# Kernel tuning notes

Measured on AMD Instinct MI355X. Metric: run time of the kernel, lower is better.

The kernel has to match this reference:

```python
import jax, jax.numpy as jnp
import numpy as np
import math

INPUT_DIM = 1024
EXPANSION = 4
SPARSITY = 0.15
ACT_SPARSITY = 0.1
OUTPUT_DIM = INPUT_DIM * EXPANSION
K = max(1, int(OUTPUT_DIM * ACT_SPARSITY))  # 409
BATCH = 16384


def setup_inputs() -> dict:
    key = jax.random.key(0)
    kx, kw, km = jax.random.split(key, 3)
    x = jax.random.normal(kx, (BATCH, INPUT_DIM), dtype=jnp.float32)
    # sparse random projection buffer, built exactly as in __init__
    w = jax.random.normal(kw, (OUTPUT_DIM, INPUT_DIM), dtype=jnp.float32)
    mask = (jax.random.uniform(km, (OUTPUT_DIM, INPUT_DIM)) < SPARSITY).astype(jnp.float32)
    scale = 1.5 / math.sqrt(INPUT_DIM * SPARSITY)
    projection_weights = w * mask * scale
    return {"x": x, "projection_weights": projection_weights}


def reference(x, projection_weights):
    # data-dependent bipolar rescale: torch uses `if x.min() >= 0`; express with where
    x_bipolar = jnp.where(x.min() >= 0, (x - 0.5) * 2.0, x)
    # [B, D_out] dense projection
    projected = jnp.einsum("bi,oi->bo", x_bipolar, projection_weights)
    # k-WTA: threshold at k-th largest value per row
    top_values, _ = jax.lax.top_k(projected, K)
    threshold = top_values[:, -1:]  # [B, 1]
    mask = (projected >= threshold).astype(projected.dtype)
    encoded = jax.nn.relu(projected) * mask
    # F.normalize(p=2, dim=1): divide by max(norm, eps)
    norm = jnp.sqrt(jnp.sum(encoded * encoded, axis=1, keepdims=True))
    return encoded / jnp.maximum(norm, 1e-12)
```

## Files before the change

### kernel.cpp

```cpp
#include <hip/hip_runtime.h>

#define BATCH   16384
#define IN_DIM  1024
#define OUT_DIM 4096
#define K_TOP   409
#define DELTA_W 6.5e-3f

typedef _Float16 half8  __attribute__((ext_vector_type(8)));
typedef _Float16 half4v __attribute__((ext_vector_type(4)));
typedef float    f32x4  __attribute__((ext_vector_type(4)));

#define WS_XH_OFF   256
#define WS_WH_OFF   (WS_XH_OFF + (size_t)BATCH * IN_DIM * 2)
#define WS_WV_OFF   (WS_WH_OFF + (size_t)OUT_DIM * IN_DIM * 2)
#define WS_WI_OFF   (WS_WV_OFF + (size_t)OUT_DIM * 256 * 4)
#define WS_WN_OFF   (WS_WI_OFF + (size_t)OUT_DIM * 256 * 2)
#define WS_NEEDED   (WS_WV_OFF)
#define WS_NEED3    (WS_WN_OFF + (size_t)OUT_DIM * 4)


__global__ __launch_bounds__(256)
void k_hasneg(const float* __restrict__ x, int n, int* __restrict__ flag) {
    const int stride = gridDim.x * blockDim.x;
    bool neg = false;
    for (int i = blockIdx.x * blockDim.x + threadIdx.x; i < n; i += stride)
        neg |= (x[i] < 0.0f);
    unsigned long long b = __ballot(neg);
    if (b != 0ULL && (threadIdx.x & 63) == 0)
        atomicOr(flag, 1);
}

__global__ __launch_bounds__(256)
void k_cvt2(const float* __restrict__ x, const float* __restrict__ w,
            _Float16* __restrict__ xh, _Float16* __restrict__ wh,
            float* __restrict__ wv, unsigned short* __restrict__ wi,
            int* __restrict__ wn, int use_csr, const int* __restrict__ flag) {
    const bool bipolar = (*flag == 0);
    const int tid = threadIdx.x;
    const int lane = tid & 63;
    const int wrow = blockIdx.x * 4 + (tid >> 6);

    const float* wr = w + (size_t)wrow * IN_DIM;
    const float4* wr4 = (const float4*)(wr + lane * 16);
    _Float16* whr = wh + (size_t)wrow * IN_DIM + lane * 16;
    float4 v[4];
    int cnt = 0;
    #pragma unroll
    for (int q = 0; q < 4; ++q) {
        v[q] = wr4[q];
        ((half4v*)whr)[q] = half4v{ (_Float16)v[q].x, (_Float16)v[q].y,
                                    (_Float16)v[q].z, (_Float16)v[q].w };
        cnt += (v[q].x != 0.0f) + (v[q].y != 0.0f)
             + (v[q].z != 0.0f) + (v[q].w != 0.0f);
    }
    if (use_csr) {
        int off = cnt;
        #pragma unroll
        for (int d = 1; d < 64; d <<= 1) {
            int t = __shfl_up(off, d);
            if (lane >= d) off += t;
        }
        const int total = __shfl(off, 63);
        off -= cnt;
        float* dv = wv + (size_t)wrow * 256;
        unsigned short* di = wi + (size_t)wrow * 256;
        int pos = off;
        #pragma unroll
        for (int q = 0; q < 4; ++q) {
            #pragma unroll
            for (int e = 0; e < 4; ++e) {
                float f = (e == 0) ? v[q].x : (e == 1) ? v[q].y
                        : (e == 2) ? v[q].z : v[q].w;
                if (f != 0.0f) {
                    dv[pos] = f;
                    di[pos] = (unsigned short)(lane * 16 + q * 4 + e);
                    ++pos;
                }
            }
        }
        if (lane == 0) {
            const int n4 = (total + 3) & ~3;
            for (int i = total; i < n4 && i < 256; ++i) { dv[i] = 0.0f; di[i] = 0; }
            wn[wrow] = total;
        }
    }

    const float4* x4 = (const float4*)x;
    half4v* xh4 = (half4v*)xh;
    const int base = blockIdx.x * 4096;
    #pragma unroll
    for (int u = 0; u < 16; ++u) {
        const int idx = base + u * 256 + tid;
        float4 xv = x4[idx];
        if (bipolar) {
            xv.x = (xv.x - 0.5f) * 2.0f; xv.y = (xv.y - 0.5f) * 2.0f;
            xv.z = (xv.z - 0.5f) * 2.0f; xv.w = (xv.w - 0.5f) * 2.0f;
        }
        xh4[idx] = half4v{ (_Float16)xv.x, (_Float16)xv.y,
                           (_Float16)xv.z, (_Float16)xv.w };
    }
}

__global__ __launch_bounds__(512, 2)
void k_gemm16(const _Float16* __restrict__ xh, const _Float16* __restrict__ wh,
              float* __restrict__ out) {
    __shared__ _Float16 Ah[2][256 * 64];
    __shared__ _Float16 Bh[2][256 * 64];
    const int tid = threadIdx.x;
    const int bm = blockIdx.x, bn = blockIdx.y;
    const int lane = tid & 63;
    const int wv = tid >> 6;
    const int wm = wv >> 2, wn = wv & 3;
    const int lr = lane & 15, lk = lane >> 4;

    const int srow = (lane >> 3);
    const int sslot = (lane & 7) ^ srow;
    f32x4 acc[8][4] = {};

    const _Float16* aS[4]; const _Float16* bS[4];
    int dOff[4];
    #pragma unroll
    for (int i = 0; i < 4; ++i) {
        const int rb = i * 64 + wv * 8;
        aS[i] = xh + (size_t)(bm * 256 + rb + srow) * IN_DIM + sslot * 8;
        bS[i] = wh + (size_t)(bn * 256 + rb + srow) * IN_DIM + sslot * 8;
        dOff[i] = rb * 64;
    }

    #pragma unroll
    for (int i = 0; i < 4; ++i) {
        __builtin_amdgcn_global_load_lds((const __attribute__((address_space(1))) void*)(aS[i]), (__attribute__((address_space(3))) void*)&Ah[0][dOff[i]], 16, 0, 0);
        __builtin_amdgcn_global_load_lds((const __attribute__((address_space(1))) void*)(bS[i]), (__attribute__((address_space(3))) void*)&Bh[0][dOff[i]], 16, 0, 0);
    }
    __syncthreads();

    int cur = 0;
    #pragma unroll 1
    for (int t = 0; t < 16; ++t) {
        if (t < 15) {
            const int kt = (t + 1) * 64;
            #pragma unroll
            for (int i = 0; i < 4; ++i) {
                __builtin_amdgcn_global_load_lds((const __attribute__((address_space(1))) void*)(aS[i] + kt), (__attribute__((address_space(3))) void*)&Ah[cur ^ 1][dOff[i]], 16, 0, 0);
                __builtin_amdgcn_global_load_lds((const __attribute__((address_space(1))) void*)(bS[i] + kt), (__attribute__((address_space(3))) void*)&Bh[cur ^ 1][dOff[i]], 16, 0, 0);
            }
        }
        #pragma unroll
        for (int h = 0; h < 2; ++h) {
            half8 bf[4];
            #pragma unroll
            for (int j = 0; j < 4; ++j) {
                const int rbv = wn * 64 + j * 16 + lr;
                const int sb = (h * 4 + lk) ^ (rbv & 7);
                bf[j] = *(const half8*)&Bh[cur][rbv * 64 + (sb << 3)];
            }
            #pragma unroll
            for (int hf = 0; hf < 2; ++hf) {
                half8 af[4];
                #pragma unroll
                for (int i = 0; i < 4; ++i) {
                    const int ra = wm * 128 + (hf * 4 + i) * 16 + lr;
                    const int sa = (h * 4 + lk) ^ (ra & 7);
                    af[i] = *(const half8*)&Ah[cur][ra * 64 + (sa << 3)];
                }
                #pragma unroll
                for (int i = 0; i < 4; ++i)
                    #pragma unroll
                    for (int j = 0; j < 4; ++j)
                        acc[hf * 4 + i][j] = __builtin_amdgcn_mfma_f32_16x16x32_f16(
                            af[i], bf[j], acc[hf * 4 + i][j], 0, 0, 0);
            }
        }
        __syncthreads();
        cur ^= 1;
    }
    #pragma unroll
    for (int i = 0; i < 8; ++i)
        #pragma unroll
        for (int j = 0; j < 4; ++j)
            #pragma unroll
            for (int q = 0; q < 4; ++q) {
                const int row = bm * 256 + wm * 128 + i * 16 + lk * 4 + q;
                const int col = bn * 256 + wn * 64 + j * 16 + lr;
                _Float16* fo = (_Float16*)((char*)out + (size_t)row * OUT_DIM * 4);
                fo[col] = (_Float16)acc[i][j][q];
            }
}

__global__ __launch_bounds__(256)
void k_self(float* __restrict__ po, const float* __restrict__ x,
            const float* __restrict__ wvals, const unsigned short* __restrict__ widx,
            const int* __restrict__ wn, const float* __restrict__ wfull,
            int use_csr, const int* __restrict__ flag) {
    __shared__ unsigned int bins[256];
    __shared__ float fred[4];
    __shared__ unsigned int wsum[4];
    __shared__ int ired[4];
    __shared__ int s_b, s_b2;
    __shared__ unsigned int s_slot, s_hi1;
    __shared__ int bcol[64];
    __shared__ float bnp[64];
    __shared__ unsigned char bsel[64];
    __shared__ float xs[IN_DIM];

    const int row = blockIdx.x;
    const int tid = threadIdx.x;
    const int lane = tid & 63, wq = tid >> 6;
    const _Float16* fr = (const _Float16*)((const char*)po + (size_t)row * OUT_DIM * 4);

    const bool bipolar = (*flag == 0);
    {
        float4 xv = ((const float4*)(x + (size_t)row * IN_DIM))[tid];
        if (bipolar) {
            xv.x = __fmul_rn(__fadd_rn(xv.x, -0.5f), 2.0f);
            xv.y = __fmul_rn(__fadd_rn(xv.y, -0.5f), 2.0f);
            xv.z = __fmul_rn(__fadd_rn(xv.z, -0.5f), 2.0f);
            xv.w = __fmul_rn(__fadd_rn(xv.w, -0.5f), 2.0f);
        }
        ((float4*)xs)[tid] = xv;
    }

    half8 h0 = *(const half8*)&fr[tid * 8];
    half8 h1 = *(const half8*)&fr[2048 + tid * 8];
    float fv[16];
    int bb[16];
    float vmax = -1e30f;
    #pragma unroll
    for (int e = 0; e < 8; ++e) {
        fv[e] = (float)h0[e];
        fv[8 + e] = (float)h1[e];
        vmax = fmaxf(vmax, fmaxf(fv[e], fv[8 + e]));
    }
    #pragma unroll
    for (int off = 32; off > 0; off >>= 1)
        vmax = fmaxf(vmax, __shfl_xor(vmax, off));
    if (lane == 0) fred[wq] = vmax;
    bins[tid] = 0;
    if (tid == 0) { s_slot = 0; s_b = 0; s_b2 = 0; s_hi1 = 0; }
    __syncthreads();
    vmax = fmaxf(fmaxf(fmaxf(fred[0], fred[1]), fmaxf(fred[2], fred[3])), 1e-6f);
    const float scale1 = 256.0f / vmax;
    const float invscale1 = vmax * (1.0f / 256.0f);

    #pragma unroll
    for (int e = 0; e < 16; ++e) {
        float f = fv[e];
        int b = -1;
        if (f > 0.0f) {
            b = (int)(f * scale1);
            if (b > 255) b = 255;
            atomicAdd(&bins[b], 1u);
        }
        bb[e] = b;
    }
    __syncthreads();
    {
        const unsigned int c = bins[255 - tid];
        unsigned int sc = c;
        #pragma unroll
        for (int off = 1; off < 64; off <<= 1) {
            unsigned int t2 = __shfl_up(sc, off);
            if (lane >= off) sc += t2;
        }
        if (lane == 63) wsum[wq] = sc;
        __syncthreads();
        for (int q = 0; q < wq; ++q) sc += wsum[q];
        if ((int)sc >= K_TOP && (int)(sc - c) < K_TOP) {
            s_b = 255 - tid;
            s_hi1 = sc - c;
        }
    }
    __syncthreads();
    const int b1 = s_b;
    const unsigned int hi1 = s_hi1;
    const float blo = (float)b1 * invscale1;
    const float scale2 = scale1 * 256.0f;
    const float s2w = invscale1 * (1.0f / 256.0f);

    bins[tid] = 0;
    __syncthreads();
    #pragma unroll
    for (int e = 0; e < 16; ++e) {
        if (bb[e] == b1) {
            int b2 = (int)((fv[e] - blo) * scale2);
            if (b2 < 0) b2 = 0;
            if (b2 > 255) b2 = 255;
            atomicAdd(&bins[b2], 1u);
        }
    }
    __syncthreads();
    {
        const unsigned int c = bins[255 - tid];
        unsigned int sc = c;
        #pragma unroll
        for (int off = 1; off < 64; off <<= 1) {
            unsigned int t2 = __shfl_up(sc, off);
            if (lane >= off) sc += t2;
        }
        if (lane == 63) wsum[wq] = sc;
        __syncthreads();
        for (int q = 0; q < wq; ++q) sc += wsum[q];
        if ((int)(hi1 + sc) >= K_TOP && (int)(hi1 + sc - c) < K_TOP)
            s_b2 = 255 - tid;
    }
    __syncthreads();
    const float thi = blo + (float)(s_b2 + 1) * s2w + DELTA_W;
    const float tlo = blo + (float)s_b2 * s2w - DELTA_W;

    int hic = 0;
    #pragma unroll
    for (int e = 0; e < 16; ++e) {
        float f = fv[e];
        if (f > thi) ++hic;
        else if (f >= tlo) {
            unsigned int p = atomicAdd(&s_slot, 1u);
            const int j = (e < 8) ? (tid * 8 + e) : (2048 + tid * 8 + e - 8);
            if (p < 64) bcol[p] = j;
        }
    }
    #pragma unroll
    for (int off = 32; off > 0; off >>= 1)
        hic += __shfl_xor(hic, off);
    if (lane == 0) ired[wq] = hic;
    __syncthreads();
    const int hi = ired[0] + ired[1] + ired[2] + ired[3];
    const int nb = (int)s_slot;
    const int nbc = nb > 64 ? 64 : nb;
    int krem = K_TOP - hi; if (krem > nb) krem = nb; if (krem < 0) krem = 0;
    const bool need = (nb != krem);

    if (need) {
        if (tid < nbc) {
            const int col = bcol[tid];
            float p = 0.0f;
            if (use_csr) {
                const int n4 = (wn[col] + 3) >> 2;
                const float4* v4 = (const float4*)(wvals + (size_t)col * 256);
                const ushort4* i4 = (const ushort4*)(widx + (size_t)col * 256);
                #pragma unroll 2
                for (int i = 0; i < n4; ++i) {
                    float4 vv = v4[i];
                    ushort4 ii = i4[i];
                    p = __fmaf_rn(xs[ii.x], vv.x, p);
                    p = __fmaf_rn(xs[ii.y], vv.y, p);
                    p = __fmaf_rn(xs[ii.z], vv.z, p);
                    p = __fmaf_rn(xs[ii.w], vv.w, p);
                }
            } else {
                const float4* wr4 = (const float4*)(wfull + (size_t)col * IN_DIM);
                const float4* xs4 = (const float4*)xs;
                #pragma unroll 4
                for (int i = 0; i < IN_DIM / 4; ++i) {
                    float4 xq = xs4[i];
                    float4 wq2 = wr4[i];
                    p = __fmaf_rn(xq.x, wq2.x, p);
                    p = __fmaf_rn(xq.y, wq2.y, p);
                    p = __fmaf_rn(xq.z, wq2.z, p);
                    p = __fmaf_rn(xq.w, wq2.w, p);
                }
            }
            bnp[tid] = p;
        }
        __syncthreads();
        if (tid < nbc) {
            const float v = bnp[tid];
            int gc = 0;
            for (int l = 0; l < nbc; ++l) gc += (bnp[l] > v);
            bsel[tid] = (gc < krem) ? 1 : 0;
        }
        __syncthreads();
    }

    float ov[16];
    float nrm2 = 0.0f;
    #pragma unroll
    for (int e = 0; e < 16; ++e) {
        float f = fv[e];
        const int j = (e < 8) ? (tid * 8 + e) : (2048 + tid * 8 + e - 8);
        bool sel = (f > thi);
        float val = f;
        if (!sel && f >= tlo) {
            if (!need) sel = true;
            else {
                for (int m = 0; m < nbc; ++m)
                    if (bcol[m] == j) {
                        sel = (bsel[m] != 0);
                        val = bnp[m];
                        break;
                    }
            }
        }
        float eo = (sel && val > 0.0f) ? val : 0.0f;
        ov[e] = eo;
        nrm2 += eo * eo;
    }
    #pragma unroll
    for (int off = 32; off > 0; off >>= 1)
        nrm2 += __shfl_xor(nrm2, off);
    if (lane == 0) fred[wq] = nrm2;
    __syncthreads();
    const float total = fred[0] + fred[1] + fred[2] + fred[3];
    const float inv = 1.0f / fmaxf(sqrtf(total), 1e-12f);

    f32x4* p4 = (f32x4*)(po + (size_t)row * OUT_DIM);
    #pragma unroll
    for (int h = 0; h < 2; ++h) {
        const int base = (h == 0) ? 0 : 8;
        const int fi = (h == 0) ? (tid * 2) : (512 + tid * 2);
        f32x4 o0 = { ov[base + 0] * inv, ov[base + 1] * inv,
                     ov[base + 2] * inv, ov[base + 3] * inv };
        f32x4 o1 = { ov[base + 4] * inv, ov[base + 5] * inv,
                     ov[base + 6] * inv, ov[base + 7] * inv };
        __builtin_nontemporal_store(o0, &p4[fi]);
        __builtin_nontemporal_store(o1, &p4[fi + 1]);
    }
}

extern "C" void kernel_launch(void* const* d_in, const int* in_sizes, int n_in,
                              void* d_out, int out_size, void* d_ws, size_t ws_size,
                              hipStream_t stream) {
    const float* x = (const float*)d_in[0];
    const float* w = (const float*)d_in[1];
    float* out = (float*)d_out;
    int* flag = (int*)d_ws;
    const int use_csr = (ws_size >= WS_NEED3) ? 1 : 0;

    hipMemsetAsync(flag, 0, sizeof(int), stream);
    k_hasneg<<<2048, 256, 0, stream>>>(x, BATCH * IN_DIM, flag);

    _Float16* xh = (_Float16*)((char*)d_ws + WS_XH_OFF);
    _Float16* wh = (_Float16*)((char*)d_ws + WS_WH_OFF);
    float* wv = (float*)((char*)d_ws + WS_WV_OFF);
    unsigned short* wi = (unsigned short*)((char*)d_ws + WS_WI_OFF);
    int* wn = (int*)((char*)d_ws + WS_WN_OFF);

    k_cvt2<<<OUT_DIM / 4, 256, 0, stream>>>(x, w, xh, wh, wv, wi, wn,
                                            use_csr, flag);
    dim3 g(BATCH / 256, OUT_DIM / 256);
    k_gemm16<<<g, 512, 0, stream>>>(xh, wh, out);

    k_self<<<BATCH, 256, 0, stream>>>(out, x, wv, wi, wn, w, use_csr, flag);
}
```

Baseline: 421.3 us.

## Shrink GEMM tile to 128x128 and use triple-buffered LDS prefetch pipeline

Rewrites the fp16 MFMA GEMM to use 128x128 block tiles with 4 waves instead of 256x256 with 8 waves, raising the block count. It replaces the double-buffered sync with a three-stage LDS ring that prefetches two k-tiles ahead, using explicit vmcnt waits and raw barriers. The aim is better latency hiding and occupancy in the GEMM. The cost is less data reuse per tile and more global traffic, and the hand-tuned waitcnt counts must match the number of outstanding loads.

```diff
diff --git a/kernel.cpp b/kernel.cpp
--- a/kernel.cpp
+++ b/kernel.cpp
@@ -101,87 +101,92 @@
     }
 }
 
-__global__ __launch_bounds__(512, 2)
+__global__ __launch_bounds__(256)
 void k_gemm16(const _Float16* __restrict__ xh, const _Float16* __restrict__ wh,
               float* __restrict__ out) {
-    __shared__ _Float16 Ah[2][256 * 64];
-    __shared__ _Float16 Bh[2][256 * 64];
+    __shared__ _Float16 Ah[3][128 * 64];
+    __shared__ _Float16 Bh[3][128 * 64];
     const int tid = threadIdx.x;
     const int bm = blockIdx.x, bn = blockIdx.y;
     const int lane = tid & 63;
     const int wv = tid >> 6;
-    const int wm = wv >> 2, wn = wv & 3;
+    const int wm = wv >> 1, wn = wv & 1;
     const int lr = lane & 15, lk = lane >> 4;
 
     const int srow = (lane >> 3);
     const int sslot = (lane & 7) ^ srow;
-    f32x4 acc[8][4] = {};
+    f32x4 acc[4][4] = {};
 
     const _Float16* aS[4]; const _Float16* bS[4];
     int dOff[4];
     #pragma unroll
     for (int i = 0; i < 4; ++i) {
-        const int rb = i * 64 + wv * 8;
-        aS[i] = xh + (size_t)(bm * 256 + rb + srow) * IN_DIM + sslot * 8;
-        bS[i] = wh + (size_t)(bn * 256 + rb + srow) * IN_DIM + sslot * 8;
+        const int rb = i * 32 + wv * 8;
+        aS[i] = xh + (size_t)(bm * 128 + rb + srow) * IN_DIM + sslot * 8;
+        bS[i] = wh + (size_t)(bn * 128 + rb + srow) * IN_DIM + sslot * 8;
         dOff[i] = rb * 64;
     }
 
     #pragma unroll
-    for (int i = 0; i < 4; ++i) {
-        __builtin_amdgcn_global_load_lds((const __attribute__((address_space(1))) void*)(aS[i]), (__attribute__((address_space(3))) void*)&Ah[0][dOff[i]], 16, 0, 0);
-        __builtin_amdgcn_global_load_lds((const __attribute__((address_space(1))) void*)(bS[i]), (__attribute__((address_space(3))) void*)&Bh[0][dOff[i]], 16, 0, 0);
-    }
-    __syncthreads();
-
-    int cur = 0;
+    for (int p = 0; p < 3; ++p) {
+        const int kt = p * 64;
+        #pragma unroll
+        for (int i = 0; i < 4; ++i) {
+            __builtin_amdgcn_global_load_lds((const __attribute__((address_space(1))) void*)(aS[i] + kt), (__attribute__((address_space(3))) void*)&Ah[p][dOff[i]], 16, 0, 0);
+            __builtin_amdgcn_global_load_lds((const __attribute__((address_space(1))) void*)(bS[i] + kt), (__attribute__((address_space(3))) void*)&Bh[p][dOff[i]], 16, 0, 0);
+        }
+    }
+    asm volatile("s_waitcnt vmcnt(16)" ::: "memory");
+    __builtin_amdgcn_s_barrier();
+    __builtin_amdgcn_sched_barrier(0);
+
     #pragma unroll 1
-    for (int t = 0; t < 16; ++t) {
-        if (t < 15) {
-            const int kt = (t + 1) * 64;
+    for (int T = 0; T < 16; ++T) {
+        const int cb = T % 3;
+        #pragma unroll
+        for (int h = 0; h < 2; ++h) {
+            half8 af[4], bf[4];
             #pragma unroll
             for (int i = 0; i < 4; ++i) {
-                __builtin_amdgcn_global_load_lds((const __attribute__((address_space(1))) void*)(aS[i] + kt), (__attribute__((address_space(3))) void*)&Ah[cur ^ 1][dOff[i]], 16, 0, 0);
-                __builtin_amdgcn_global_load_lds((const __attribute__((address_space(1))) void*)(bS[i] + kt), (__attribute__((address_space(3))) void*)&Bh[cur ^ 1][dOff[i]], 16, 0, 0);
-            }
-        }
-        #pragma unroll
-        for (int h = 0; h < 2; ++h) {
-            half8 bf[4];
+                const int ra = wm * 64 + i * 16 + lr;
+                const int sa = (h * 4 + lk) ^ (ra & 7);
+                af[i] = *(const half8*)&Ah[cb][ra * 64 + (sa << 3)];
+                const int rb = wn * 64 + i * 16 + lr;
+                const int sb = (h * 4 + lk) ^ (rb & 7);
+                bf[i] = *(const half8*)&Bh[cb][rb * 64 + (sb << 3)];
+            }
             #pragma unroll
-            for (int j = 0; j < 4; ++j) {
-                const int rbv = wn * 64 + j * 16 + lr;
-                const int sb = (h * 4 + lk) ^ (rbv & 7);
-                bf[j] = *(const half8*)&Bh[cur][rbv * 64 + (sb << 3)];
-            }
+            for (int i = 0; i < 4; ++i)
+                #pragma unroll
+                for (int j = 0; j < 4; ++j)
+                    acc[i][j] = __builtin_amdgcn_mfma_f32_16x16x32_f16(
+                        af[i], bf[j], acc[i][j], 0, 0, 0);
+        }
+        __builtin_amdgcn_sched_barrier(0);
+        if (T < 14) {
+            asm volatile("s_waitcnt vmcnt(8)" ::: "memory");
+        } else {
+            asm volatile("s_waitcnt vmcnt(0)" ::: "memory");
+        }
+        __builtin_amdgcn_s_barrier();
+        __builtin_amdgcn_sched_barrier(0);
+        if (T + 3 <= 15) {
+            const int kt = (T + 3) * 64;
             #pragma unroll
-            for (int hf = 0; hf < 2; ++hf) {
-                half8 af[4];
-                #pragma unroll
-                for (int i = 0; i < 4; ++i) {
-                    const int ra = wm * 128 + (hf * 4 + i) * 16 + lr;
-                    const int sa = (h * 4 + lk) ^ (ra & 7);
-                    af[i] = *(const half8*)&Ah[cur][ra * 64 + (sa << 3)];
-                }
-                #pragma unroll
-                for (int i = 0; i < 4; ++i)
-                    #pragma unroll
-                    for (int j = 0; j < 4; ++j)
-                        acc[hf * 4 + i][j] = __builtin_amdgcn_mfma_f32_16x16x32_f16(
-                            af[i], bf[j], acc[hf * 4 + i][j], 0, 0, 0);
-            }
-        }
-        __syncthreads();
-        cur ^= 1;
-    }
-    #pragma unroll
-    for (int i = 0; i < 8; ++i)
+            for (int i = 0; i < 4; ++i) {
+                __builtin_amdgcn_global_load_lds((const __attribute__((address_space(1))) void*)(aS[i] + kt), (__attribute__((address_space(3))) void*)&Ah[cb][dOff[i]], 16, 0, 0);
+                __builtin_amdgcn_global_load_lds((const __attribute__((address_space(1))) void*)(bS[i] + kt), (__attribute__((address_space(3))) void*)&Bh[cb][dOff[i]], 16, 0, 0);
+            }
+        }
+    }
+    #pragma unroll
+    for (int i = 0; i < 4; ++i)
         #pragma unroll
         for (int j = 0; j < 4; ++j)
             #pragma unroll
             for (int q = 0; q < 4; ++q) {
-                const int row = bm * 256 + wm * 128 + i * 16 + lk * 4 + q;
-                const int col = bn * 256 + wn * 64 + j * 16 + lr;
+                const int row = bm * 128 + wm * 64 + i * 16 + lk * 4 + q;
+                const int col = bn * 128 + wn * 64 + j * 16 + lr;
                 _Float16* fo = (_Float16*)((char*)out + (size_t)row * OUT_DIM * 4);
                 fo[col] = (_Float16)acc[i][j][q];
             }
@@ -436,8 +441,8 @@
 
     k_cvt2<<<OUT_DIM / 4, 256, 0, stream>>>(x, w, xh, wh, wv, wi, wn,
                                             use_csr, flag);
-    dim3 g(BATCH / 256, OUT_DIM / 256);
-    k_gemm16<<<g, 512, 0, stream>>>(xh, wh, out);
+    dim3 g(BATCH / 128, OUT_DIM / 128);
+    k_gemm16<<<g, 256, 0, stream>>>(xh, wh, out);
 
     k_self<<<BATCH, 256, 0, stream>>>(out, x, wv, wi, wn, w, use_csr, flag);
 }
```

After: 575.3 us. 1.37x slower.
